# Performance work log

Hardware: AMD Instinct MI355X
Metric: run time of the kernel (lower is better)

The kernel has to match this reference:

```python
import jax, jax.numpy as jnp
import numpy as np

EPS = 1e-7
N, L, BATCH = 512, 2, 128
N_IPF = 10


def setup_inputs() -> dict:
    key = jax.random.key(0)
    k1, k2, k3, k4 = jax.random.split(key, 4)
    return {
        "x": jax.random.randint(k1, (BATCH, N), 0, L, dtype=jnp.int32),
        "W": jax.random.normal(k2, (N, N), dtype=jnp.float32),
        "V_compress": jax.random.normal(k3, (N, L), dtype=jnp.float32),
        "E_compress": jax.random.normal(k4, (N, N, L, L), dtype=jnp.float32),
    }


def _moat_forward(W, V_compress, E_compress, x):
    n, l = V_compress.shape
    # marginals / joints
    V = jax.nn.softmax(V_compress, axis=1)              # (n, l)
    E = jnp.exp(E_compress)                              # (n, n, l, l)
    E = E / E.sum(axis=(-2, -1), keepdims=True)

    # 10-step Sinkhorn / IPF projection onto marginals V
    A_b = V[:, None, :, None]                            # (n, 1, l, 1)
    B_b = V[None, :, None, :]                            # (1, n, 1, l)
    for _ in range(N_IPF):
        row_marg = E.sum(axis=3, keepdims=True) + EPS    # (n, n, l, 1)
        col_marg = E.sum(axis=2, keepdims=True) + EPS    # (n, n, 1, l)
        E = E * (A_b / row_marg)
        E = E * (B_b / col_marg)
        E = E / (E.sum(axis=(-2, -1), keepdims=True) + EPS)

    # zero the diagonal (i == j) pairwise joints, clamp
    E = E * (1.0 - jnp.eye(n, dtype=E.dtype))[:, :, None, None]
    E = jnp.clip(E, 0.0, 1.0)

    # symmetric edge-weight matrix from strictly-lower-triangular sigmoid(W)
    Wm = jax.nn.sigmoid(W)
    Wm = jnp.tril(Wm, k=-1)
    Wm = Wm.T + Wm                                       # (n, n), zero diag
    L_0 = -Wm + jnp.diag(Wm.sum(axis=1))                 # graph Laplacian

    idx = jnp.arange(n)
    # Pr[b, i] = V[i, x[b, i]]
    Pr = V[idx[None, :], x]                              # (batch, n)
    # P[b, i, j] = E[i, j, x[b, i], x[b, j]]
    P = E[idx[None, :, None], idx[None, None, :], x[:, :, None], x[:, None, :]]  # (batch, n, n)
    P = P / (Pr[:, :, None] * Pr[:, None, :])

    WP = Wm[None, :, :] * P                              # (batch, n, n)
    Lb = -WP + jax.vmap(jnp.diag)(WP.sum(axis=2))        # batched Laplacian

    # matrix-tree theorem: logdet of the (n-1, n-1) principal minor
    _, logdet_L = jnp.linalg.slogdet(Lb[:, 1:, 1:])
    _, logdet_L0 = jnp.linalg.slogdet(L_0[1:, 1:])
    return jnp.log(Pr).sum(axis=1) + logdet_L - logdet_L0  # (batch,)


def reference(x, W, V_compress, E_compress):
    return _moat_forward(W, V_compress, E_compress, x)
```

## Files before the change

### kernel.cpp

```cpp
#include <hip/hip_runtime.h>
#include <hip/hip_bf16.h>
#include <math.h>

#define NDIM 512
#define NB   128
#define NMAT 129
#define EPSF 1e-7f
#define MS  ((size_t)262144)
#define LTS ((size_t)32768)
#define PSTR ((size_t)524288)

#define OFF_E   ((size_t)0)
#define OFF_WM  ((size_t)1048576)
#define OFF_V   ((size_t)(OFF_WM + 262144))
#define OFF_IPR ((size_t)(OFF_V + 1024))
#define OFF_LPR ((size_t)(OFF_IPR + 65536))
#define OFF_LD  ((size_t)(OFF_LPR + 128))
#define OFF_LT  ((size_t)1377792)
#define OFF_MAT ((size_t)(OFF_LT + (size_t)NMAT*LTS))

__device__ __forceinline__ float rdlane(float v, int l) {
  return __uint_as_float((unsigned)__builtin_amdgcn_readlane((int)__float_as_uint(v), l));
}

__global__ __launch_bounds__(256) void k_V(const float* __restrict__ Vc, float* __restrict__ V) {
  int i = blockIdx.x * 256 + threadIdx.x;
  if (i < NDIM) {
    float v0 = Vc[2*i], v1 = Vc[2*i+1];
    float mx = fmaxf(v0, v1);
    float e0 = expf(v0 - mx), e1 = expf(v1 - mx);
    float s = e0 + e1;
    V[2*i]   = e0 / s;
    V[2*i+1] = e1 / s;
  }
}

__global__ __launch_bounds__(256) void k_Wm(const float* __restrict__ W, float* __restrict__ Wm) {
  int idx = blockIdx.x * 256 + threadIdx.x;
  int i = idx >> 9, j = idx & 511;
  float v = 0.f;
  if (i > j)      v = 1.f / (1.f + expf(-W[i*NDIM + j]));
  else if (i < j) v = 1.f / (1.f + expf(-W[j*NDIM + i]));
  Wm[idx] = v;
}

__global__ __launch_bounds__(256) void k_E(const float* __restrict__ Ec, const float* __restrict__ V,
                                           float* __restrict__ E2) {
  int idx = blockIdx.x * 256 + threadIdx.x;
  int i = idx >> 9, j = idx & 511;
  float4 ec = reinterpret_cast<const float4*>(Ec)[idx];
  float e00 = expf(ec.x), e01 = expf(ec.y), e10 = expf(ec.z), e11 = expf(ec.w);
  float s = e00 + e01 + e10 + e11;
  float inv = 1.f / s;
  e00 *= inv; e01 *= inv; e10 *= inv; e11 *= inv;
  float A0 = V[2*i], A1 = V[2*i+1];
  float B0 = V[2*j], B1 = V[2*j+1];
  for (int t = 0; t < 10; ++t) {
    float rm0 = e00 + e01 + EPSF, rm1 = e10 + e11 + EPSF;
    float cm0 = e00 + e10 + EPSF, cm1 = e01 + e11 + EPSF;
    float f0 = A0 / rm0, f1 = A1 / rm1;
    e00 *= f0; e01 *= f0; e10 *= f1; e11 *= f1;
    float g0 = B0 / cm0, g1 = B1 / cm1;
    e00 *= g0; e10 *= g0; e01 *= g1; e11 *= g1;
    float ss = e00 + e01 + e10 + e11 + EPSF;
    float iv = 1.f / ss;
    e00 *= iv; e01 *= iv; e10 *= iv; e11 *= iv;
  }
  if (i == j) { e00 = 0.f; e01 = 0.f; e10 = 0.f; e11 = 0.f; }
  e00 = fminf(fmaxf(e00, 0.f), 1.f);
  e01 = fminf(fmaxf(e01, 0.f), 1.f);
  e10 = fminf(fmaxf(e10, 0.f), 1.f);
  e11 = fminf(fmaxf(e11, 0.f), 1.f);
  reinterpret_cast<float2*>(E2)[idx]               = make_float2(e00, e01);
  reinterpret_cast<float2*>(E2 + PSTR)[idx]        = make_float2(e10, e11);
}

__global__ __launch_bounds__(256) void k_Pr(const int* __restrict__ x, const float* __restrict__ V,
                                            float* __restrict__ invPr, float* __restrict__ logPr) {
  const int b = blockIdx.x;
  const int tid = threadIdx.x;
  float acc = 0.f;
  for (int ii = tid; ii < NDIM; ii += 256) {
    const int xv = x[b*NDIM + ii];
    const float p = V[2*ii + xv];
    invPr[b*NDIM + ii] = 1.f / p;
    acc += logf(p);
  }
  for (int off = 32; off > 0; off >>= 1) acc += __shfl_down(acc, off, 64);
  __shared__ float sw[4];
  if ((tid & 63) == 0) sw[tid >> 6] = acc;
  __syncthreads();
  if (tid == 0) logPr[b] = sw[0] + sw[1] + sw[2] + sw[3];
}

__global__ __launch_bounds__(512) void k_build(const int* __restrict__ x, const float* __restrict__ E2,
                                               const float* __restrict__ Wm, const float* __restrict__ invPr,
                                               float* __restrict__ Mall) {
  const int b = blockIdx.x;
  const int i = blockIdx.y*8 + (threadIdx.x >> 6);
  const int lane = threadIdx.x & 63;
  const int j0 = lane << 3;

  const float4 w0 = *(const float4*)(Wm + (size_t)i*NDIM + j0);
  const float4 w1 = *(const float4*)(Wm + (size_t)i*NDIM + j0 + 4);
  float wp[8];
  if (b < NB) {
    const int   xi   = x[b*NDIM + i];
    const float ipri = invPr[b*NDIM + i];
    const int4  xa = *(const int4*)(x + b*NDIM + j0);
    const int4  xb = *(const int4*)(x + b*NDIM + j0 + 4);
    const float4 pa = *(const float4*)(invPr + b*NDIM + j0);
    const float4 pb = *(const float4*)(invPr + b*NDIM + j0 + 4);
    const float* pl = E2 + (size_t)xi*PSTR + ((size_t)i*NDIM + j0)*2;
    const float4 ea = *(const float4*)(pl);
    const float4 eb = *(const float4*)(pl + 4);
    const float4 ec = *(const float4*)(pl + 8);
    const float4 ed = *(const float4*)(pl + 12);
    wp[0] = w0.x * (xa.x ? ea.y : ea.x) * pa.x;
    wp[1] = w0.y * (xa.y ? ea.w : ea.z) * pa.y;
    wp[2] = w0.z * (xa.z ? eb.y : eb.x) * pa.z;
    wp[3] = w0.w * (xa.w ? eb.w : eb.z) * pa.w;
    wp[4] = w1.x * (xb.x ? ec.y : ec.x) * pb.x;
    wp[5] = w1.y * (xb.y ? ec.w : ec.z) * pb.y;
    wp[6] = w1.z * (xb.z ? ed.y : ed.x) * pb.z;
    wp[7] = w1.w * (xb.w ? ed.w : ed.z) * pb.w;
    #pragma unroll
    for (int k = 0; k < 8; ++k) wp[k] *= ipri;
  } else {
    wp[0]=w0.x; wp[1]=w0.y; wp[2]=w0.z; wp[3]=w0.w;
    wp[4]=w1.x; wp[5]=w1.y; wp[6]=w1.z; wp[7]=w1.w;
  }
  float s = ((wp[0]+wp[1])+(wp[2]+wp[3])) + ((wp[4]+wp[5])+(wp[6]+wp[7]));
  #pragma unroll
  for (int off = 32; off > 0; off >>= 1) s += __shfl_xor(s, off, 64);

  float o[8];
  #pragma unroll
  for (int k = 0; k < 8; ++k) o[k] = -wp[k];
  if (i == 0) {
    #pragma unroll
    for (int k = 0; k < 8; ++k) o[k] = 0.f;
    if (lane == 0) o[0] = 1.f;
  } else {
    if (lane == 0) o[0] = 0.f;
    #pragma unroll
    for (int k = 0; k < 8; ++k)
      if (j0 + k == i) o[k] = s;
  }
  float* dst = Mall + (size_t)b*MS + (size_t)i*NDIM + j0;
  *(float4*)(dst)   = make_float4(o[0],o[1],o[2],o[3]);
  *(float4*)(dst+4) = make_float4(o[4],o[5],o[6],o[7]);
}

template<int KK>
struct WFact {
  static __device__ __forceinline__ void run(float (&a)[64], const int lane,
                                             float& mypiv, float& myrec) {
    const float piv = rdlane(a[KK], KK);
    const float rec = 1.0f / piv;
    if (lane == KK) { mypiv = piv; myrec = rec; }
    if (lane > KK) {
      const float l = a[KK] * rec;
      a[KK] = l;
      #pragma unroll
      for (int c = KK + 1; c < 64; ++c)
        a[c] -= l * rdlane(a[c], KK);
    }
    WFact<KK + 1>::run(a, lane, mypiv, myrec);
  }
};
template<>
struct WFact<64> {
  static __device__ __forceinline__ void run(float (&)[64], int, float&, float&) {}
};

template<int C>
struct SolveStep {
  static __device__ __forceinline__ void run(float (&a)[64], const float (*T)[72]) {
    float acc = a[C];
    #pragma unroll
    for (int p = 0; p < C; ++p)
      acc -= a[p] * T[C][p];
    a[C] = acc * T[C][66];
    SolveStep<C + 1>::run(a, T);
  }
};
template<>
struct SolveStep<64> {
  static __device__ __forceinline__ void run(float (&)[64], const float (*)[72]) {}
};

__global__ __launch_bounds__(512) void k_panel(float* __restrict__ Mall, float* __restrict__ Lt,
                                               float* __restrict__ logdets, int k0, int mrem) {
  const int b = blockIdx.x;
  float* __restrict__ M = Mall + (size_t)b*MS;
  float* __restrict__ L = Lt + (size_t)b*LTS;
  const int t = threadIdx.x;
  const int m = NDIM - k0;
  __shared__ float T[64][72];

  float a[64];
  if (t < m) {
    const float* row = M + (size_t)(k0+t)*NDIM + k0;
    #pragma unroll
    for (int c4 = 0; c4 < 16; ++c4) {
      float4 v = *(const float4*)(row + c4*4);
      a[c4*4+0]=v.x; a[c4*4+1]=v.y; a[c4*4+2]=v.z; a[c4*4+3]=v.w;
    }
  }

  if (t < 64) {
    float mypiv = 1.f, myrec = 1.f;
    WFact<0>::run(a, t, mypiv, myrec);
    #pragma unroll
    for (int c = 0; c < 64; ++c) T[c][t] = a[c];
    T[t][66] = myrec;
    float v = logf(fabsf(mypiv));
    #pragma unroll
    for (int off = 32; off > 0; off >>= 1) v += __shfl_down(v, off, 64);
    if (t == 0) logdets[b] = (k0 == 0) ? v : (logdets[b] + v);
  }
  __syncthreads();

  if (mrem > 0) {
    if (t >= 64 && t < m) {
      SolveStep<0>::run(a, T);
      #pragma unroll
      for (int c = 0; c < 64; ++c) L[(size_t)c*NDIM + t] = a[c];
    }
    if (t < mrem) {
      const int col = k0 + 64 + t;
      float u[64];
      #pragma unroll
      for (int r = 0; r < 64; ++r) u[r] = M[(size_t)(k0+r)*NDIM + col];
      #pragma unroll
      for (int p = 0; p < 63; ++p) {
        const float lv = u[p];
        #pragma unroll
        for (int kk = p+1; kk < 64; ++kk)
          u[kk] -= T[p][kk] * lv;
      }
      #pragma unroll
      for (int r = 1; r < 64; ++r) M[(size_t)(k0+r)*NDIM + col] = u[r];
    }
  }
}

__global__ __launch_bounds__(256, 4) void k_gemm(float* __restrict__ Mall, const float* __restrict__ Lt,
                                                 int k0) {
  const int b = blockIdx.x;
  float* __restrict__ M = Mall + (size_t)b*MS;
  const float* __restrict__ L = Lt + (size_t)b*LTS;
  __shared__ float As[64][68];
  __shared__ float Bs[64][68];
  const int tid = threadIdx.x;
  const int tx = tid & 15, ty = tid >> 4;
  const int rowbase = 64 + blockIdx.y*64;
  const int colbase = 64 + blockIdx.z*64;
  #pragma unroll
  for (int i = 0; i < 4; ++i) {
    int q = tid + 256*i;
    int p = q >> 4, f = q & 15;
    *(float4*)&As[p][f*4] = *(const float4*)&L[(size_t)p*NDIM + rowbase + f*4];
    *(float4*)&Bs[p][f*4] = *(const float4*)&M[(size_t)(k0+p)*NDIM + (k0+colbase) + f*4];
  }
  float* Crow = M + (size_t)(k0+rowbase+ty*4)*NDIM + (k0+colbase+tx*4);
  float4 c0 = *(float4*)(Crow + 0*NDIM);
  float4 c1 = *(float4*)(Crow + 1*NDIM);
  float4 c2 = *(float4*)(Crow + 2*NDIM);
  float4 c3 = *(float4*)(Crow + 3*NDIM);
  __syncthreads();
  #pragma unroll
  for (int p = 0; p < 64; ++p) {
    const float4 av = *(const float4*)&As[p][ty*4];
    const float4 bv = *(const float4*)&Bs[p][tx*4];
    c0.x -= av.x*bv.x; c0.y -= av.x*bv.y; c0.z -= av.x*bv.z; c0.w -= av.x*bv.w;
    c1.x -= av.y*bv.x; c1.y -= av.y*bv.y; c1.z -= av.y*bv.z; c1.w -= av.y*bv.w;
    c2.x -= av.z*bv.x; c2.y -= av.z*bv.y; c2.z -= av.z*bv.z; c2.w -= av.z*bv.w;
    c3.x -= av.w*bv.x; c3.y -= av.w*bv.y; c3.z -= av.w*bv.z; c3.w -= av.w*bv.w;
  }
  *(float4*)(Crow + 0*NDIM) = c0;
  *(float4*)(Crow + 1*NDIM) = c1;
  *(float4*)(Crow + 2*NDIM) = c2;
  *(float4*)(Crow + 3*NDIM) = c3;
}

__global__ void k_final(const float* __restrict__ logPr, const float* __restrict__ logdets,
                        float* __restrict__ out) {
  int t = threadIdx.x;
  if (t < NB) out[t] = logPr[t] + logdets[t] - logdets[NB];
}

extern "C" void kernel_launch(void* const* d_in, const int* in_sizes, int n_in,
                              void* d_out, int out_size, void* d_ws, size_t ws_size,
                              hipStream_t stream) {
  const int*   x  = (const int*)  d_in[0];
  const float* W  = (const float*)d_in[1];
  const float* Vc = (const float*)d_in[2];
  const float* Ec = (const float*)d_in[3];
  float* out = (float*)d_out;
  float* ws  = (float*)d_ws;
  (void)in_sizes; (void)n_in; (void)out_size; (void)ws_size;

  float* Mat = ws + OFF_MAT;
  float* Lt  = ws + OFF_LT;
  float* Ld  = ws + OFF_LD;

  k_V  <<<2,    256, 0, stream>>>(Vc, ws + OFF_V);
  k_Wm <<<1024, 256, 0, stream>>>(W,  ws + OFF_WM);
  k_E  <<<1024, 256, 0, stream>>>(Ec, ws + OFF_V, ws + OFF_E);
  k_Pr <<<NB,   256, 0, stream>>>(x,  ws + OFF_V, ws + OFF_IPR, ws + OFF_LPR);
  dim3 gb(NMAT, 64);
  k_build<<<gb, 512, 0, stream>>>(x, ws + OFF_E, ws + OFF_WM, ws + OFF_IPR, Mat);

  for (int s = 0; s < 8; ++s) {
    const int k0 = s*64;
    const int mrem = NDIM - k0 - 64;
    k_panel<<<NMAT, 512, 0, stream>>>(Mat, Lt, Ld, k0, mrem);
    if (mrem > 0) {
      const int nt = mrem/64;
      dim3 gg(NMAT, nt, nt);
      k_gemm<<<gg, 256, 0, stream>>>(Mat, Lt, k0);
    }
  }
  k_final<<<1, 128, 0, stream>>>(ws + OFF_LPR, Ld, out);
}
```

Measured before the change: 628.1 us.

## Fuse prep kernels, recompute softmax inline, vectorize panel LDS reads

Merges the V-softmax, sigmoid edge-weight and Sinkhorn kernels into one prep kernel. The softmax is recomputed inline in both the prep and Pr kernels, which removes two launches and the V buffer. The panel kernel's triangular solve and trailing-column update now read the shared T tile with float4 loads, and the tile row stride is shrunk to 68 with 16-byte alignment. The workspace layout is also reordered so the matrices come before the L panels. The cost is redundant exp work per element, plus a T[t][66] slot that now sits inside the padded row.

```diff
diff --git a/kernel.cpp b/kernel.cpp
--- a/kernel.cpp
+++ b/kernel.cpp
@@ -12,49 +12,40 @@
 
 #define OFF_E   ((size_t)0)
 #define OFF_WM  ((size_t)1048576)
-#define OFF_V   ((size_t)(OFF_WM + 262144))
-#define OFF_IPR ((size_t)(OFF_V + 1024))
-#define OFF_LPR ((size_t)(OFF_IPR + 65536))
-#define OFF_LD  ((size_t)(OFF_LPR + 128))
-#define OFF_LT  ((size_t)1377792)
-#define OFF_MAT ((size_t)(OFF_LT + (size_t)NMAT*LTS))
+#define OFF_IPR ((size_t)1310720)
+#define OFF_LPR ((size_t)1376256)
+#define OFF_LD  ((size_t)1376384)
+#define OFF_MAT ((size_t)1377792)
+#define OFF_LT  ((size_t)(OFF_MAT + (size_t)NMAT*MS))
 
 __device__ __forceinline__ float rdlane(float v, int l) {
   return __uint_as_float((unsigned)__builtin_amdgcn_readlane((int)__float_as_uint(v), l));
 }
 
-__global__ __launch_bounds__(256) void k_V(const float* __restrict__ Vc, float* __restrict__ V) {
-  int i = blockIdx.x * 256 + threadIdx.x;
-  if (i < NDIM) {
-    float v0 = Vc[2*i], v1 = Vc[2*i+1];
-    float mx = fmaxf(v0, v1);
-    float e0 = expf(v0 - mx), e1 = expf(v1 - mx);
-    float s = e0 + e1;
-    V[2*i]   = e0 / s;
-    V[2*i+1] = e1 / s;
-  }
-}
-
-__global__ __launch_bounds__(256) void k_Wm(const float* __restrict__ W, float* __restrict__ Wm) {
+__global__ __launch_bounds__(256) void k_prep(const float* __restrict__ W, const float* __restrict__ Vc,
+                                              const float* __restrict__ Ec, float* __restrict__ Wm,
+                                              float* __restrict__ E2) {
   int idx = blockIdx.x * 256 + threadIdx.x;
   int i = idx >> 9, j = idx & 511;
-  float v = 0.f;
-  if (i > j)      v = 1.f / (1.f + expf(-W[i*NDIM + j]));
-  else if (i < j) v = 1.f / (1.f + expf(-W[j*NDIM + i]));
-  Wm[idx] = v;
-}
-
-__global__ __launch_bounds__(256) void k_E(const float* __restrict__ Ec, const float* __restrict__ V,
-                                           float* __restrict__ E2) {
-  int idx = blockIdx.x * 256 + threadIdx.x;
-  int i = idx >> 9, j = idx & 511;
+  float wv = 0.f;
+  if (i > j)      wv = 1.f / (1.f + expf(-W[i*NDIM + j]));
+  else if (i < j) wv = 1.f / (1.f + expf(-W[j*NDIM + i]));
+  Wm[idx] = wv;
+  float vi0 = Vc[2*i], vi1 = Vc[2*i+1];
+  float mi = fmaxf(vi0, vi1);
+  float ei0 = expf(vi0 - mi), ei1 = expf(vi1 - mi);
+  float si = ei0 + ei1;
+  float A0 = ei0 / si, A1 = ei1 / si;
+  float vj0 = Vc[2*j], vj1 = Vc[2*j+1];
+  float mj = fmaxf(vj0, vj1);
+  float ej0 = expf(vj0 - mj), ej1 = expf(vj1 - mj);
+  float sj = ej0 + ej1;
+  float B0 = ej0 / sj, B1 = ej1 / sj;
   float4 ec = reinterpret_cast<const float4*>(Ec)[idx];
   float e00 = expf(ec.x), e01 = expf(ec.y), e10 = expf(ec.z), e11 = expf(ec.w);
   float s = e00 + e01 + e10 + e11;
   float inv = 1.f / s;
   e00 *= inv; e01 *= inv; e10 *= inv; e11 *= inv;
-  float A0 = V[2*i], A1 = V[2*i+1];
-  float B0 = V[2*j], B1 = V[2*j+1];
   for (int t = 0; t < 10; ++t) {
     float rm0 = e00 + e01 + EPSF, rm1 = e10 + e11 + EPSF;
     float cm0 = e00 + e10 + EPSF, cm1 = e01 + e11 + EPSF;
@@ -71,18 +62,22 @@
   e01 = fminf(fmaxf(e01, 0.f), 1.f);
   e10 = fminf(fmaxf(e10, 0.f), 1.f);
   e11 = fminf(fmaxf(e11, 0.f), 1.f);
-  reinterpret_cast<float2*>(E2)[idx]               = make_float2(e00, e01);
-  reinterpret_cast<float2*>(E2 + PSTR)[idx]        = make_float2(e10, e11);
-}
-
-__global__ __launch_bounds__(256) void k_Pr(const int* __restrict__ x, const float* __restrict__ V,
+  reinterpret_cast<float2*>(E2)[idx]        = make_float2(e00, e01);
+  reinterpret_cast<float2*>(E2 + PSTR)[idx] = make_float2(e10, e11);
+}
+
+__global__ __launch_bounds__(256) void k_Pr(const int* __restrict__ x, const float* __restrict__ Vc,
                                             float* __restrict__ invPr, float* __restrict__ logPr) {
   const int b = blockIdx.x;
   const int tid = threadIdx.x;
   float acc = 0.f;
   for (int ii = tid; ii < NDIM; ii += 256) {
     const int xv = x[b*NDIM + ii];
-    const float p = V[2*ii + xv];
+    float v0 = Vc[2*ii], v1 = Vc[2*ii+1];
+    float mx = fmaxf(v0, v1);
+    float e0 = expf(v0 - mx), e1 = expf(v1 - mx);
+    float s = e0 + e1;
+    const float p = xv ? (e1 / s) : (e0 / s);
     invPr[b*NDIM + ii] = 1.f / p;
     acc += logf(p);
   }
@@ -176,18 +171,26 @@
 
 template<int C>
 struct SolveStep {
-  static __device__ __forceinline__ void run(float (&a)[64], const float (*T)[72]) {
+  static __device__ __forceinline__ void run(float (&a)[64], const float (*T)[68]) {
+    const float* Trow = T[C];
     float acc = a[C];
     #pragma unroll
-    for (int p = 0; p < C; ++p)
-      acc -= a[p] * T[C][p];
-    a[C] = acc * T[C][66];
+    for (int p4 = 0; p4 + 4 <= C; p4 += 4) {
+      const float4 tv = *(const float4*)(Trow + p4);
+      acc -= a[p4+0] * tv.x;
+      acc -= a[p4+1] * tv.y;
+      acc -= a[p4+2] * tv.z;
+      acc -= a[p4+3] * tv.w;
+    }
+    #pragma unroll
+    for (int p = C & ~3; p < C; ++p) acc -= a[p] * Trow[p];
+    a[C] = acc * Trow[66];
     SolveStep<C + 1>::run(a, T);
   }
 };
 template<>
 struct SolveStep<64> {
-  static __device__ __forceinline__ void run(float (&)[64], const float (*)[72]) {}
+  static __device__ __forceinline__ void run(float (&)[64], const float (*)[68]) {}
 };
 
 __global__ __launch_bounds__(512) void k_panel(float* __restrict__ Mall, float* __restrict__ Lt,
@@ -197,7 +200,7 @@
   float* __restrict__ L = Lt + (size_t)b*LTS;
   const int t = threadIdx.x;
   const int m = NDIM - k0;
-  __shared__ float T[64][72];
+  __shared__ __align__(16) float T[64][68];
 
   float a[64];
   if (t < m) {
@@ -236,9 +239,19 @@
       #pragma unroll
       for (int p = 0; p < 63; ++p) {
         const float lv = u[p];
+        const float* Trow = T[p];
+        const int kk0 = p + 1;
+        const int kkA = (p + 4) & ~3;
         #pragma unroll
-        for (int kk = p+1; kk < 64; ++kk)
-          u[kk] -= T[p][kk] * lv;
+        for (int kk = kk0; kk < kkA; ++kk) u[kk] -= Trow[kk] * lv;
+        #pragma unroll
+        for (int kk4 = kkA; kk4 < 64; kk4 += 4) {
+          const float4 tv = *(const float4*)(Trow + kk4);
+          u[kk4+0] -= tv.x * lv;
+          u[kk4+1] -= tv.y * lv;
+          u[kk4+2] -= tv.z * lv;
+          u[kk4+3] -= tv.w * lv;
+        }
       }
       #pragma unroll
       for (int r = 1; r < 64; ++r) M[(size_t)(k0+r)*NDIM + col] = u[r];
@@ -251,8 +264,8 @@
   const int b = blockIdx.x;
   float* __restrict__ M = Mall + (size_t)b*MS;
   const float* __restrict__ L = Lt + (size_t)b*LTS;
-  __shared__ float As[64][68];
-  __shared__ float Bs[64][68];
+  __shared__ __align__(16) float As[64][68];
+  __shared__ __align__(16) float Bs[64][68];
   const int tid = threadIdx.x;
   const int tx = tid & 15, ty = tid >> 4;
   const int rowbase = 64 + blockIdx.y*64;
@@ -306,10 +319,8 @@
   float* Lt  = ws + OFF_LT;
   float* Ld  = ws + OFF_LD;
 
-  k_V  <<<2,    256, 0, stream>>>(Vc, ws + OFF_V);
-  k_Wm <<<1024, 256, 0, stream>>>(W,  ws + OFF_WM);
-  k_E  <<<1024, 256, 0, stream>>>(Ec, ws + OFF_V, ws + OFF_E);
-  k_Pr <<<NB,   256, 0, stream>>>(x,  ws + OFF_V, ws + OFF_IPR, ws + OFF_LPR);
+  k_prep<<<1024, 256, 0, stream>>>(W, Vc, Ec, ws + OFF_WM, ws + OFF_E);
+  k_Pr  <<<NB,   256, 0, stream>>>(x, Vc, ws + OFF_IPR, ws + OFF_LPR);
   dim3 gb(NMAT, 64);
   k_build<<<gb, 512, 0, stream>>>(x, ws + OFF_E, ws + OFF_WM, ws + OFF_IPR, Mat);
 
```

Result: faster. 614.8 us (-2.1%).
